# Performance work log

Measured on AMD Instinct MI355X. Metric: run time of the kernel, lower is better.

## Reference

```python
import jax, jax.numpy as jnp
import numpy as np

N_HEADS = 16
HEAD_DIM = 128


def _rotate_half(x):
    x1, x2 = jnp.split(x, 2, axis=-1)
    return jnp.concatenate((-x2, x1), axis=-1)


def setup_inputs() -> dict:
    key = jax.random.key(0)
    ks = jax.random.split(key, 6)
    B, T, D = 2, 2048, 2048
    d = D // N_HEADS  # 128
    x = jax.random.normal(ks[0], (B, T, D), dtype=jnp.float32)
    # RoPE tables (shape [1,1,T,head_dim]) built as in standard implementations
    inv_freq = 1.0 / (10000.0 ** (jnp.arange(0, d, 2, dtype=jnp.float32) / d))
    ang = jnp.arange(T, dtype=jnp.float32)[:, None] * inv_freq[None, :]  # [T, d/2]
    emb = jnp.concatenate((ang, ang), axis=-1)  # [T, d]
    rope_cos = jnp.cos(emb)[None, None]
    rope_sin = jnp.sin(emb)[None, None]
    qkv_w = jax.random.normal(ks[1], (3 * D, D), dtype=jnp.float32) * (1.0 / np.sqrt(D))
    qkv_b = jnp.zeros((3 * D,), dtype=jnp.float32)
    out_w = jax.random.normal(ks[2], (D, D), dtype=jnp.float32) * (1.0 / np.sqrt(D))
    out_b = jnp.zeros((D,), dtype=jnp.float32)
    return {"x": x, "rope_cos": rope_cos, "rope_sin": rope_sin,
            "qkv_w": qkv_w, "qkv_b": qkv_b, "out_w": out_w, "out_b": out_b}


def reference(x, rope_cos, rope_sin, qkv_w, qkv_b, out_w, out_b):
    B, T, D = x.shape
    H, d = N_HEADS, D // N_HEADS
    # fused QKV projection: [B,T,3D] -> [3,B,H,T,d]
    qkv = (jnp.einsum('btd,ed->bte', x, qkv_w) + qkv_b)
    qkv = qkv.reshape(B, T, 3, H, d).transpose(2, 0, 3, 1, 4)
    q, k, v = qkv[0], qkv[1], qkv[2]
    cos = rope_cos[:, :, :T, :].astype(q.dtype)
    sin = rope_sin[:, :, :T, :].astype(q.dtype)
    q = q * cos + _rotate_half(q) * sin
    k = k * cos + _rotate_half(k) * sin
    # causal SDPA
    scale = 1.0 / jnp.sqrt(jnp.array(d, dtype=q.dtype))
    scores = jnp.einsum('bhqd,bhkd->bhqk', q, k) * scale  # [B,H,T,T]
    causal = jnp.tril(jnp.ones((T, T), dtype=bool))
    scores = jnp.where(causal, scores, jnp.finfo(scores.dtype).min)
    attn = jax.nn.softmax(scores, axis=-1)
    out = jnp.einsum('bhqk,bhkd->bhqd', attn, v)  # [B,H,T,d]
    out = out.transpose(0, 2, 1, 3).reshape(B, T, D)
    return jnp.einsum('btd,ed->bte', out, out_w) + out_b
```

## Files before the change

### kernel.cpp

```cpp
#include <hip/hip_runtime.h>
#include <cstdint>
#include <cstddef>

typedef unsigned short u16;
using bf16x8 = __attribute__((ext_vector_type(8))) short;
using f32x4  = __attribute__((ext_vector_type(4))) float;

#define MFMA16(a, b, c) __builtin_amdgcn_mfma_f32_16x16x32_bf16((a), (b), (c), 0, 0, 0)

__device__ __forceinline__ u16 f2bf(float f) {
  union { float f; unsigned u; } x; x.f = f;
  unsigned r = x.u + 0x7fffu + ((x.u >> 16) & 1u);
  return (u16)(r >> 16);
}
__device__ __forceinline__ float bf2f(u16 h) {
  union { unsigned u; float f; } x; x.u = ((unsigned)h) << 16;
  return x.f;
}
__device__ __forceinline__ void gll16(const void* g, void* l) {
  __builtin_amdgcn_global_load_lds((const __attribute__((address_space(1))) void*)g,
                                   (__attribute__((address_space(3))) void*)l, 16, 0, 0);
}

union U8 { bf16x8 v; u16 u[8]; };

__global__ __launch_bounds__(256) void cvt_kernel(const float* __restrict__ in,
                                                  u16* __restrict__ out, int n4) {
  int i = blockIdx.x * blockDim.x + threadIdx.x;
  if (i >= n4) return;
  float4 v = ((const float4*)in)[i];
  ushort4 o;
  o.x = f2bf(v.x); o.y = f2bf(v.y); o.z = f2bf(v.z); o.w = f2bf(v.w);
  ((ushort4*)out)[i] = o;
}

__global__ __launch_bounds__(256) void gemm_bt(const u16* __restrict__ A,
                                               const u16* __restrict__ Bw,
                                               const float* __restrict__ bias,
                                               void* __restrict__ Cout,
                                               int M, int N, int K, int out_bf16) {
  __shared__ u16 As[128 * 32];
  __shared__ u16 Bs[128 * 32];
  const int tid = threadIdx.x;
  const int lane = tid & 63, wave = tid >> 6;
  const int col = lane & 15, quad = lane >> 4;
  const int wr = wave >> 1, wc = wave & 1;
  const int bm = blockIdx.y, bn = blockIdx.x;
  const u16* Ag = A + (size_t)bm * 128 * K;
  const u16* Bg = Bw + (size_t)bn * 128 * K;
  f32x4 acc[4][4] = {};
  const int r0 = tid >> 2, kc = (tid & 3) * 8;
  for (int k0 = 0; k0 < K; k0 += 32) {
    __syncthreads();
    gll16(Ag + (size_t)r0 * K + k0 + kc,        (void*)(As + (size_t)tid * 8));
    gll16(Ag + (size_t)(r0 + 64) * K + k0 + kc, (void*)(As + (size_t)(256 + tid) * 8));
    gll16(Bg + (size_t)r0 * K + k0 + kc,        (void*)(Bs + (size_t)tid * 8));
    gll16(Bg + (size_t)(r0 + 64) * K + k0 + kc, (void*)(Bs + (size_t)(256 + tid) * 8));
    __syncthreads();
    bf16x8 af[4], bf[4];
#pragma unroll
    for (int i = 0; i < 4; i++) {
      af[i] = *(const bf16x8*)&As[(wr * 64 + i * 16 + col) * 32 + quad * 8];
      bf[i] = *(const bf16x8*)&Bs[(wc * 64 + i * 16 + col) * 32 + quad * 8];
    }
#pragma unroll
    for (int i = 0; i < 4; i++)
#pragma unroll
      for (int j = 0; j < 4; j++)
        acc[i][j] = MFMA16(af[i], bf[j], acc[i][j]);
  }
#pragma unroll
  for (int i = 0; i < 4; i++) {
    int row0 = bm * 128 + wr * 64 + i * 16 + quad * 4;
#pragma unroll
    for (int j = 0; j < 4; j++) {
      int cn = bn * 128 + wc * 64 + j * 16 + col;
      float bv = bias[cn];
#pragma unroll
      for (int r = 0; r < 4; r++) {
        float v = acc[i][j][r] + bv;
        size_t off = (size_t)(row0 + r) * N + cn;
        if (out_bf16) ((u16*)Cout)[off] = f2bf(v);
        else          ((float*)Cout)[off] = v;
      }
    }
  }
}

__global__ __launch_bounds__(256) void rope_kernel(const u16* __restrict__ qkv,
                                                   const float* __restrict__ cosT,
                                                   const float* __restrict__ sinT,
                                                   u16* __restrict__ qo,
                                                   u16* __restrict__ ko,
                                                   u16* __restrict__ vt) {
  __shared__ u16 vs[128 * 72];
  const int bh = blockIdx.x;
  const int b = bh >> 4, h = bh & 15;
  const int tb = blockIdx.y;
  const int tid = threadIdx.x;
  const int tl = tid >> 2;
  const int g = tid & 3;
  const int t = tb * 64 + tl;
  const size_t qrow = ((size_t)(b * 2048 + t)) * 6144 + h * 128;
  const size_t orow = ((size_t)bh * 2048 + t) * 128;
  const int tt = t * 128;
  const int dl = g * 16, dh = 64 + dl;
  const float scale = 0.08838834764831845f;
#pragma unroll
  for (int cch = 0; cch < 2; cch++) {
    const int o8 = cch * 8;
    U8 ql, qh, kl, kh, vl, vh;
    ql.v = *(const bf16x8*)&qkv[qrow + dl + o8];
    qh.v = *(const bf16x8*)&qkv[qrow + dh + o8];
    kl.v = *(const bf16x8*)&qkv[qrow + 2048 + dl + o8];
    kh.v = *(const bf16x8*)&qkv[qrow + 2048 + dh + o8];
    vl.v = *(const bf16x8*)&qkv[qrow + 4096 + dl + o8];
    vh.v = *(const bf16x8*)&qkv[qrow + 4096 + dh + o8];
    float cl[8], ch_[8], sl[8], sh_[8];
    *(float4*)&cl[0]  = *(const float4*)&cosT[tt + dl + o8];
    *(float4*)&cl[4]  = *(const float4*)&cosT[tt + dl + o8 + 4];
    *(float4*)&ch_[0] = *(const float4*)&cosT[tt + dh + o8];
    *(float4*)&ch_[4] = *(const float4*)&cosT[tt + dh + o8 + 4];
    *(float4*)&sl[0]  = *(const float4*)&sinT[tt + dl + o8];
    *(float4*)&sl[4]  = *(const float4*)&sinT[tt + dl + o8 + 4];
    *(float4*)&sh_[0] = *(const float4*)&sinT[tt + dh + o8];
    *(float4*)&sh_[4] = *(const float4*)&sinT[tt + dh + o8 + 4];
    U8 aq, bq, ak, bk;
#pragma unroll
    for (int i = 0; i < 8; i++) {
      float qlf = bf2f(ql.u[i]), qhf = bf2f(qh.u[i]);
      float klf = bf2f(kl.u[i]), khf = bf2f(kh.u[i]);
      aq.u[i] = f2bf((qlf * cl[i]  - qhf * sl[i])  * scale);
      bq.u[i] = f2bf((qhf * ch_[i] + qlf * sh_[i]) * scale);
      ak.u[i] = f2bf(klf * cl[i]  - khf * sl[i]);
      bk.u[i] = f2bf(khf * ch_[i] + klf * sh_[i]);
    }
    *(bf16x8*)&qo[orow + dl + o8] = aq.v;
    *(bf16x8*)&qo[orow + dh + o8] = bq.v;
    *(bf16x8*)&ko[orow + dl + o8] = ak.v;
    *(bf16x8*)&ko[orow + dh + o8] = bk.v;
#pragma unroll
    for (int i = 0; i < 8; i++) {
      vs[(dl + o8 + i) * 72 + tl] = vl.u[i];
      vs[(dh + o8 + i) * 72 + tl] = vh.u[i];
    }
  }
  __syncthreads();
#pragma unroll
  for (int c = 0; c < 4; c++) {
    int idx = c * 256 + tid;
    int dd = idx >> 3, chk = idx & 7;
    bf16x8 vv = *(const bf16x8*)&vs[dd * 72 + chk * 8];
    *(bf16x8*)&vt[((size_t)bh * 128 + dd) * 2048 + tb * 64 + chk * 8] = vv;
  }
}

__global__ __launch_bounds__(256) void attn_kernel(const u16* __restrict__ Q,
                                                   const u16* __restrict__ Kk,
                                                   const u16* __restrict__ Vt,
                                                   u16* __restrict__ O) {
  __shared__ u16 Ks[64 * 136];
  __shared__ u16 Vs[128 * 72];
  __shared__ u16 Ps[4][16 * 72];
  const int bh = blockIdx.y, b = bh >> 4, h = bh & 15;
  const int qtile = gridDim.x - 1 - blockIdx.x;
  const int qb = qtile * 128;
  const int tid = threadIdx.x, wave = tid >> 6, lane = tid & 63;
  const int col = lane & 15, quad = lane >> 4;
  const int qw0 = qb + wave * 32;
  const int qw1 = qw0 + 16;
  const u16* Qg = Q + (size_t)bh * 2048 * 128;
  const u16* Kg = Kk + (size_t)bh * 2048 * 128;
  const u16* Vg = Vt + (size_t)bh * 128 * 2048;
  bf16x8 qf0[4], qf1[4];
#pragma unroll
  for (int c = 0; c < 4; c++) {
    qf0[c] = *(const bf16x8*)&Qg[(size_t)(qw0 + col) * 128 + c * 32 + quad * 8];
    qf1[c] = *(const bf16x8*)&Qg[(size_t)(qw1 + col) * 128 + c * 32 + quad * 8];
  }
  f32x4 o0[8] = {}, o1[8] = {};
  float ls0[4] = {0.f, 0.f, 0.f, 0.f}, ls1[4] = {0.f, 0.f, 0.f, 0.f};
  const int ntiles = (qb + 128) >> 6;
  const int kr = tid >> 2, kc = (tid & 3) * 8;
  const int vr = tid >> 1, vc = (tid & 1) * 8;
  for (int it = 0; it < ntiles; ++it) {
    const int kt = it << 6;
    __syncthreads();
#pragma unroll
    for (int u = 0; u < 4; u++)
      *(bf16x8*)&Ks[kr * 136 + kc + u * 32] =
          *(const bf16x8*)&Kg[(size_t)(kt + kr) * 128 + kc + u * 32];
#pragma unroll
    for (int u = 0; u < 4; u++)
      *(bf16x8*)&Vs[vr * 72 + vc + u * 16] =
          *(const bf16x8*)&Vg[(size_t)vr * 2048 + kt + vc + u * 16];
    __syncthreads();
    if (kt > qw1 + 15) continue;
    const bool do0 = (kt <= qw0 + 15);
    f32x4 s0[4] = {}, s1[4] = {};
#pragma unroll
    for (int c = 0; c < 4; c++) {
#pragma unroll
      for (int kg = 0; kg < 4; kg++) {
        bf16x8 kf = *(const bf16x8*)&Ks[(kg * 16 + col) * 136 + c * 32 + quad * 8];
        s0[kg] = MFMA16(qf0[c], kf, s0[kg]);
        s1[kg] = MFMA16(qf1[c], kf, s1[kg]);
      }
    }
    u16* pw = Ps[wave];
    if (do0) {
#pragma unroll
      for (int kg = 0; kg < 4; kg++)
#pragma unroll
        for (int r = 0; r < 4; r++) {
          int key = kt + kg * 16 + col, qg = qw0 + quad * 4 + r;
          float p = (key <= qg) ? __expf(s0[kg][r]) : 0.f;
          ls0[r] += p;
          pw[(quad * 4 + r) * 72 + kg * 16 + col] = f2bf(p);
        }
#pragma unroll
      for (int ks = 0; ks < 64; ks += 32) {
        bf16x8 pf = *(const bf16x8*)&pw[col * 72 + ks + quad * 8];
#pragma unroll
        for (int dt = 0; dt < 8; dt++) {
          bf16x8 vf = *(const bf16x8*)&Vs[(dt * 16 + col) * 72 + ks + quad * 8];
          o0[dt] = MFMA16(pf, vf, o0[dt]);
        }
      }
    }
    {
#pragma unroll
      for (int kg = 0; kg < 4; kg++)
#pragma unroll
        for (int r = 0; r < 4; r++) {
          int key = kt + kg * 16 + col, qg = qw1 + quad * 4 + r;
          float p = (key <= qg) ? __expf(s1[kg][r]) : 0.f;
          ls1[r] += p;
          pw[(quad * 4 + r) * 72 + kg * 16 + col] = f2bf(p);
        }
#pragma unroll
      for (int ks = 0; ks < 64; ks += 32) {
        bf16x8 pf = *(const bf16x8*)&pw[col * 72 + ks + quad * 8];
#pragma unroll
        for (int dt = 0; dt < 8; dt++) {
          bf16x8 vf = *(const bf16x8*)&Vs[(dt * 16 + col) * 72 + ks + quad * 8];
          o1[dt] = MFMA16(pf, vf, o1[dt]);
        }
      }
    }
  }
#pragma unroll
  for (int st = 1; st < 16; st <<= 1)
#pragma unroll
    for (int r = 0; r < 4; r++) {
      ls0[r] += __shfl_xor(ls0[r], st);
      ls1[r] += __shfl_xor(ls1[r], st);
    }
#pragma unroll
  for (int r = 0; r < 4; r++) {
    float inv0 = 1.0f / ls0[r], inv1 = 1.0f / ls1[r];
    size_t row0 = ((size_t)(b * 2048 + qw0 + quad * 4 + r)) * 2048 + h * 128;
    size_t row1 = ((size_t)(b * 2048 + qw1 + quad * 4 + r)) * 2048 + h * 128;
#pragma unroll
    for (int dt = 0; dt < 8; dt++) {
      O[row0 + dt * 16 + col] = f2bf(o0[dt][r] * inv0);
      O[row1 + dt * 16 + col] = f2bf(o1[dt][r] * inv1);
    }
  }
}

extern "C" void kernel_launch(void* const* d_in, const int* in_sizes, int n_in,
                              void* d_out, int out_size, void* d_ws, size_t ws_size,
                              hipStream_t stream) {
  const float* x        = (const float*)d_in[0];
  const float* rope_cos = (const float*)d_in[1];
  const float* rope_sin = (const float*)d_in[2];
  const float* qkv_w    = (const float*)d_in[3];
  const float* qkv_b    = (const float*)d_in[4];
  const float* out_w    = (const float*)d_in[5];
  const float* out_b    = (const float*)d_in[6];
  float* out = (float*)d_out;
  u16* ws = (u16*)d_ws;
  u16* xb    = ws;
  u16* wqkvb = xb + 8388608;
  u16* woutb = wqkvb + 12582912;
  u16* qkvb  = woutb + 4194304;
  u16* qb    = qkvb + 25165824;
  u16* kb    = qb + 8388608;
  u16* vtb   = kb + 8388608;
  u16* attnb = xb;

  cvt_kernel<<<8192, 256, 0, stream>>>(x, xb, 2097152);
  cvt_kernel<<<12288, 256, 0, stream>>>(qkv_w, wqkvb, 3145728);
  cvt_kernel<<<4096, 256, 0, stream>>>(out_w, woutb, 1048576);
  gemm_bt<<<dim3(48, 32), 256, 0, stream>>>(xb, wqkvb, qkv_b, qkvb, 4096, 6144, 2048, 1);
  rope_kernel<<<dim3(32, 32), 256, 0, stream>>>(qkvb, rope_cos, rope_sin, qb, kb, vtb);
  attn_kernel<<<dim3(16, 32), 256, 0, stream>>>(qb, kb, vtb, attnb);
  gemm_bt<<<dim3(16, 32), 256, 0, stream>>>(attnb, woutb, out_b, out, 4096, 2048, 2048, 0);
}
```

Baseline: 470.4 us.

## Rewrite GEMM as 256x256 tile, triple-buffered, swizzled LDS, 8-wave kernel

Result: no change. 473.0 us (+0.6%).

```diff
diff --git a/kernel.cpp b/kernel.cpp
--- a/kernel.cpp
+++ b/kernel.cpp
@@ -34,48 +34,98 @@
   ((ushort4*)out)[i] = o;
 }
 
-__global__ __launch_bounds__(256) void gemm_bt(const u16* __restrict__ A,
-                                               const u16* __restrict__ Bw,
-                                               const float* __restrict__ bias,
-                                               void* __restrict__ Cout,
-                                               int M, int N, int K, int out_bf16) {
-  __shared__ u16 As[128 * 32];
-  __shared__ u16 Bs[128 * 32];
+__global__ __launch_bounds__(512, 2) void gemm_bt256(const u16* __restrict__ A,
+                                                     const u16* __restrict__ Bw,
+                                                     const float* __restrict__ bias,
+                                                     void* __restrict__ Cout,
+                                                     int M, int N, int K, int out_bf16) {
+  __shared__ u16 As[3][8192];
+  __shared__ u16 Bs[3][8192];
   const int tid = threadIdx.x;
   const int lane = tid & 63, wave = tid >> 6;
   const int col = lane & 15, quad = lane >> 4;
-  const int wr = wave >> 1, wc = wave & 1;
+  const int wr = wave >> 2, wc = wave & 3;
   const int bm = blockIdx.y, bn = blockIdx.x;
-  const u16* Ag = A + (size_t)bm * 128 * K;
-  const u16* Bg = Bw + (size_t)bn * 128 * K;
-  f32x4 acc[4][4] = {};
-  const int r0 = tid >> 2, kc = (tid & 3) * 8;
-  for (int k0 = 0; k0 < K; k0 += 32) {
-    __syncthreads();
-    gll16(Ag + (size_t)r0 * K + k0 + kc,        (void*)(As + (size_t)tid * 8));
-    gll16(Ag + (size_t)(r0 + 64) * K + k0 + kc, (void*)(As + (size_t)(256 + tid) * 8));
-    gll16(Bg + (size_t)r0 * K + k0 + kc,        (void*)(Bs + (size_t)tid * 8));
-    gll16(Bg + (size_t)(r0 + 64) * K + k0 + kc, (void*)(Bs + (size_t)(256 + tid) * 8));
-    __syncthreads();
-    bf16x8 af[4], bf[4];
+  const u16* Ag = A + (size_t)bm * 256 * K;
+  const u16* Bg = Bw + (size_t)bn * 256 * K;
+  const int r0 = tid >> 2, r1 = (tid + 512) >> 2;
+  const int sl = tid & 3;
+  const size_t off0 = (size_t)r0 * K + ((sl ^ ((r0 >> 1) & 3)) << 3);
+  const size_t off1 = (size_t)r1 * K + ((sl ^ ((r1 >> 1) & 3)) << 3);
+  f32x4 acc[8][4] = {};
+  const int NT = K >> 5;
+
+#define STAGE_A(buf, k0) do { \
+    gll16(Ag + off0 + (k0), (void*)(As[buf] + tid * 8)); \
+    gll16(Ag + off1 + (k0), (void*)(As[buf] + 4096 + tid * 8)); } while (0)
+#define STAGE_B(buf, k0) do { \
+    gll16(Bg + off0 + (k0), (void*)(Bs[buf] + tid * 8)); \
+    gll16(Bg + off1 + (k0), (void*)(Bs[buf] + 4096 + tid * 8)); } while (0)
+
+  STAGE_A(0, 0); STAGE_B(0, 0);
+  if (NT > 1) {
+    STAGE_A(1, 32); STAGE_B(1, 32);
+    asm volatile("s_waitcnt vmcnt(4)" ::: "memory");
+  } else {
+    asm volatile("s_waitcnt vmcnt(0)" ::: "memory");
+  }
+  __builtin_amdgcn_s_barrier();
+
+  int cur = 0;
+  for (int t = 0; t < NT; ++t) {
+    const u16* Ab = As[cur];
+    const u16* Bb = Bs[cur];
+    int nx2 = cur + 2; if (nx2 >= 3) nx2 -= 3;
+    const bool pf = (t + 2) < NT;
+    const int k2 = (t + 2) << 5;
+    bf16x8 af[4], bfr[4];
 #pragma unroll
     for (int i = 0; i < 4; i++) {
-      af[i] = *(const bf16x8*)&As[(wr * 64 + i * 16 + col) * 32 + quad * 8];
-      bf[i] = *(const bf16x8*)&Bs[(wc * 64 + i * 16 + col) * 32 + quad * 8];
-    }
+      const int row = wr * 128 + i * 16 + col;
+      af[i] = *(const bf16x8*)&Ab[row * 32 + ((quad ^ ((row >> 1) & 3)) << 3)];
+    }
+#pragma unroll
+    for (int j = 0; j < 4; j++) {
+      const int row = wc * 64 + j * 16 + col;
+      bfr[j] = *(const bf16x8*)&Bb[row * 32 + ((quad ^ ((row >> 1) & 3)) << 3)];
+    }
+    if (pf) STAGE_A(nx2, k2);
+    __builtin_amdgcn_s_barrier();
+    __builtin_amdgcn_s_setprio(1);
 #pragma unroll
     for (int i = 0; i < 4; i++)
 #pragma unroll
       for (int j = 0; j < 4; j++)
-        acc[i][j] = MFMA16(af[i], bf[j], acc[i][j]);
-  }
-#pragma unroll
-  for (int i = 0; i < 4; i++) {
-    int row0 = bm * 128 + wr * 64 + i * 16 + quad * 4;
+        acc[i][j] = MFMA16(af[i], bfr[j], acc[i][j]);
+    __builtin_amdgcn_s_setprio(0);
+    __builtin_amdgcn_s_barrier();
+#pragma unroll
+    for (int i = 0; i < 4; i++) {
+      const int row = wr * 128 + (i + 4) * 16 + col;
+      af[i] = *(const bf16x8*)&Ab[row * 32 + ((quad ^ ((row >> 1) & 3)) << 3)];
+    }
+    if (pf) STAGE_B(nx2, k2);
+    __builtin_amdgcn_s_barrier();
+    __builtin_amdgcn_s_setprio(1);
+#pragma unroll
+    for (int i = 0; i < 4; i++)
+#pragma unroll
+      for (int j = 0; j < 4; j++)
+        acc[4 + i][j] = MFMA16(af[i], bfr[j], acc[4 + i][j]);
+    __builtin_amdgcn_s_setprio(0);
+    if (pf) asm volatile("s_waitcnt vmcnt(4)" ::: "memory");
+    else    asm volatile("s_waitcnt vmcnt(0)" ::: "memory");
+    __builtin_amdgcn_s_barrier();
+    cur = (cur + 1 == 3) ? 0 : cur + 1;
+  }
+
+#pragma unroll
+  for (int i = 0; i < 8; i++) {
+    const int row0 = bm * 256 + wr * 128 + i * 16 + quad * 4;
 #pragma unroll
     for (int j = 0; j < 4; j++) {
-      int cn = bn * 128 + wc * 64 + j * 16 + col;
-      float bv = bias[cn];
+      const int cn = bn * 256 + wc * 64 + j * 16 + col;
+      const float bv = bias[cn];
 #pragma unroll
       for (int r = 0; r < 4; r++) {
         float v = acc[i][j][r] + bv;
@@ -85,6 +135,8 @@
       }
     }
   }
+#undef STAGE_A
+#undef STAGE_B
 }
 
 __global__ __launch_bounds__(256) void rope_kernel(const u16* __restrict__ qkv,
@@ -293,8 +345,8 @@
   cvt_kernel<<<8192, 256, 0, stream>>>(x, xb, 2097152);
   cvt_kernel<<<12288, 256, 0, stream>>>(qkv_w, wqkvb, 3145728);
   cvt_kernel<<<4096, 256, 0, stream>>>(out_w, woutb, 1048576);
-  gemm_bt<<<dim3(48, 32), 256, 0, stream>>>(xb, wqkvb, qkv_b, qkvb, 4096, 6144, 2048, 1);
+  gemm_bt256<<<dim3(24, 16), 512, 0, stream>>>(xb, wqkvb, qkv_b, qkvb, 4096, 6144, 2048, 1);
   rope_kernel<<<dim3(32, 32), 256, 0, stream>>>(qkvb, rope_cos, rope_sin, qb, kb, vtb);
   attn_kernel<<<dim3(16, 32), 256, 0, stream>>>(qb, kb, vtb, attnb);
-  gemm_bt<<<dim3(16, 32), 256, 0, stream>>>(attnb, woutb, out_b, out, 4096, 2048, 2048, 0);
-}
+  gemm_bt256<<<dim3(8, 16), 512, 0, stream>>>(attnb, woutb, out_b, out, 4096, 2048, 2048, 0);
+}
```

## Replace GEMM with 256x256-tile, 4-stage pipelined, LDS-swizzled MFMA kernel

Applied to the files above, without the earlier changes.

Measured after the change: 448.8 us. 1.05x faster.

```diff
diff --git a/kernel.cpp b/kernel.cpp
--- a/kernel.cpp
+++ b/kernel.cpp
@@ -34,48 +34,102 @@
   ((ushort4*)out)[i] = o;
 }
 
-__global__ __launch_bounds__(256) void gemm_bt(const u16* __restrict__ A,
-                                               const u16* __restrict__ Bw,
-                                               const float* __restrict__ bias,
-                                               void* __restrict__ Cout,
-                                               int M, int N, int K, int out_bf16) {
-  __shared__ u16 As[128 * 32];
-  __shared__ u16 Bs[128 * 32];
+__global__ __launch_bounds__(512, 2) void gemm_bt256(const u16* __restrict__ A,
+                                                     const u16* __restrict__ Bw,
+                                                     const float* __restrict__ bias,
+                                                     void* __restrict__ Cout,
+                                                     int M, int N, int K, int out_bf16) {
+  __shared__ u16 As[4][8192];
+  __shared__ u16 Bs[4][8192];
   const int tid = threadIdx.x;
   const int lane = tid & 63, wave = tid >> 6;
   const int col = lane & 15, quad = lane >> 4;
-  const int wr = wave >> 1, wc = wave & 1;
+  const int wr = wave >> 2, wc = wave & 3;
   const int bm = blockIdx.y, bn = blockIdx.x;
-  const u16* Ag = A + (size_t)bm * 128 * K;
-  const u16* Bg = Bw + (size_t)bn * 128 * K;
-  f32x4 acc[4][4] = {};
-  const int r0 = tid >> 2, kc = (tid & 3) * 8;
-  for (int k0 = 0; k0 < K; k0 += 32) {
-    __syncthreads();
-    gll16(Ag + (size_t)r0 * K + k0 + kc,        (void*)(As + (size_t)tid * 8));
-    gll16(Ag + (size_t)(r0 + 64) * K + k0 + kc, (void*)(As + (size_t)(256 + tid) * 8));
-    gll16(Bg + (size_t)r0 * K + k0 + kc,        (void*)(Bs + (size_t)tid * 8));
-    gll16(Bg + (size_t)(r0 + 64) * K + k0 + kc, (void*)(Bs + (size_t)(256 + tid) * 8));
-    __syncthreads();
-    bf16x8 af[4], bf[4];
-#pragma unroll
-    for (int i = 0; i < 4; i++) {
-      af[i] = *(const bf16x8*)&As[(wr * 64 + i * 16 + col) * 32 + quad * 8];
-      bf[i] = *(const bf16x8*)&Bs[(wc * 64 + i * 16 + col) * 32 + quad * 8];
-    }
-#pragma unroll
-    for (int i = 0; i < 4; i++)
-#pragma unroll
-      for (int j = 0; j < 4; j++)
-        acc[i][j] = MFMA16(af[i], bf[j], acc[i][j]);
-  }
+  const u16* Ag = A + (size_t)bm * 256 * K;
+  const u16* Bg = Bw + (size_t)bn * 256 * K;
+  const int r0 = tid >> 2, r1 = (tid + 512) >> 2;
+  const int sl = tid & 3;
+  const size_t off0 = (size_t)r0 * K + ((sl ^ ((r0 >> 1) & 3)) << 3);
+  const size_t off1 = (size_t)r1 * K + ((sl ^ ((r1 >> 1) & 3)) << 3);
+  f32x4 acc[8][4] = {};
+  const int NT = K >> 5;
+  int ra1[4], ra2[4], rb[4];
 #pragma unroll
   for (int i = 0; i < 4; i++) {
-    int row0 = bm * 128 + wr * 64 + i * 16 + quad * 4;
+    int r1_ = wr * 128 + i * 16 + col;
+    int r2_ = r1_ + 64;
+    int rb_ = wc * 64 + i * 16 + col;
+    ra1[i] = r1_ * 32 + ((quad ^ ((r1_ >> 1) & 3)) << 3);
+    ra2[i] = r2_ * 32 + ((quad ^ ((r2_ >> 1) & 3)) << 3);
+    rb[i]  = rb_ * 32 + ((quad ^ ((rb_ >> 1) & 3)) << 3);
+  }
+
+#define STAGE_A(bi, k0) do { \
+    gll16(Ag + off0 + (k0), (void*)(As[bi] + tid * 8)); \
+    gll16(Ag + off1 + (k0), (void*)(As[bi] + 4096 + tid * 8)); } while (0)
+#define STAGE_B(bi, k0) do { \
+    gll16(Bg + off0 + (k0), (void*)(Bs[bi] + tid * 8)); \
+    gll16(Bg + off1 + (k0), (void*)(Bs[bi] + 4096 + tid * 8)); } while (0)
+
+#define TILE_STEP(AF, BF, AFN, BFN, TT)                                        \
+  do {                                                                         \
+    const u16* Ab_ = As[(TT) & 3];                                             \
+    _Pragma("unroll")                                                          \
+    for (int i_ = 0; i_ < 4; i_++) af2[i_] = *(const bf16x8*)&Ab_[ra2[i_]];    \
+    if ((TT) + 2 < NT) STAGE_A(((TT) + 2) & 3, ((TT) + 2) << 5);               \
+    __builtin_amdgcn_s_setprio(1);                                             \
+    _Pragma("unroll")                                                          \
+    for (int i_ = 0; i_ < 4; i_++)                                             \
+      _Pragma("unroll")                                                        \
+      for (int j_ = 0; j_ < 4; j_++)                                           \
+        acc[i_][j_] = MFMA16(AF[i_], BF[j_], acc[i_][j_]);                     \
+    __builtin_amdgcn_s_setprio(0);                                             \
+    if ((TT) + 2 < NT) { asm volatile("s_waitcnt vmcnt(2)" ::: "memory"); }    \
+    else               { asm volatile("s_waitcnt vmcnt(0)" ::: "memory"); }    \
+    __builtin_amdgcn_s_barrier();                                              \
+    if ((TT) + 1 < NT) {                                                       \
+      const u16* An_ = As[((TT) + 1) & 3];                                     \
+      const u16* Bn_ = Bs[((TT) + 1) & 3];                                     \
+      _Pragma("unroll")                                                        \
+      for (int i_ = 0; i_ < 4; i_++) {                                         \
+        AFN[i_] = *(const bf16x8*)&An_[ra1[i_]];                               \
+        BFN[i_] = *(const bf16x8*)&Bn_[rb[i_]];                                \
+      }                                                                        \
+    }                                                                          \
+    if ((TT) + 2 < NT) STAGE_B(((TT) + 2) & 3, ((TT) + 2) << 5);               \
+    __builtin_amdgcn_s_setprio(1);                                             \
+    _Pragma("unroll")                                                          \
+    for (int i_ = 0; i_ < 4; i_++)                                             \
+      _Pragma("unroll")                                                        \
+      for (int j_ = 0; j_ < 4; j_++)                                           \
+        acc[4 + i_][j_] = MFMA16(af2[i_], BF[j_], acc[4 + i_][j_]);            \
+    __builtin_amdgcn_s_setprio(0);                                             \
+  } while (0)
+
+  STAGE_A(0, 0); STAGE_B(0, 0); STAGE_A(1, 32);
+  asm volatile("s_waitcnt vmcnt(2)" ::: "memory");
+  __builtin_amdgcn_s_barrier();
+  bf16x8 afX[4], bfX[4], afY[4], bfY[4], af2[4];
+#pragma unroll
+  for (int i = 0; i < 4; i++) {
+    afX[i] = *(const bf16x8*)&As[0][ra1[i]];
+    bfX[i] = *(const bf16x8*)&Bs[0][rb[i]];
+  }
+  STAGE_B(1, 32);
+
+  for (int t = 0; t < NT; t += 2) {
+    TILE_STEP(afX, bfX, afY, bfY, t);
+    TILE_STEP(afY, bfY, afX, bfX, t + 1);
+  }
+
+#pragma unroll
+  for (int i = 0; i < 8; i++) {
+    const int row0 = bm * 256 + wr * 128 + i * 16 + quad * 4;
 #pragma unroll
     for (int j = 0; j < 4; j++) {
-      int cn = bn * 128 + wc * 64 + j * 16 + col;
-      float bv = bias[cn];
+      const int cn = bn * 256 + wc * 64 + j * 16 + col;
+      const float bv = bias[cn];
 #pragma unroll
       for (int r = 0; r < 4; r++) {
         float v = acc[i][j][r] + bv;
@@ -85,6 +139,9 @@
       }
     }
   }
+#undef STAGE_A
+#undef STAGE_B
+#undef TILE_STEP
 }
 
 __global__ __launch_bounds__(256) void rope_kernel(const u16* __restrict__ qkv,
@@ -293,8 +350,8 @@
   cvt_kernel<<<8192, 256, 0, stream>>>(x, xb, 2097152);
   cvt_kernel<<<12288, 256, 0, stream>>>(qkv_w, wqkvb, 3145728);
   cvt_kernel<<<4096, 256, 0, stream>>>(out_w, woutb, 1048576);
-  gemm_bt<<<dim3(48, 32), 256, 0, stream>>>(xb, wqkvb, qkv_b, qkvb, 4096, 6144, 2048, 1);
+  gemm_bt256<<<dim3(24, 16), 512, 0, stream>>>(xb, wqkvb, qkv_b, qkvb, 4096, 6144, 2048, 1);
   rope_kernel<<<dim3(32, 32), 256, 0, stream>>>(qkvb, rope_cos, rope_sin, qb, kb, vtb);
   attn_kernel<<<dim3(16, 32), 256, 0, stream>>>(qb, kb, vtb, attnb);
-  gemm_bt<<<dim3(16, 32), 256, 0, stream>>>(attnb, woutb, out_b, out, 4096, 2048, 2048, 0);
-}
+  gemm_bt256<<<dim3(8, 16), 512, 0, stream>>>(attnb, woutb, out_b, out, 4096, 2048, 2048, 0);
+}
```

## Replace GEMM with 256x256 double-buffered 8-wave pipelined kernel with swizzled LDS

Applied to the files above, without the earlier changes.

Result: faster. 452.4 us (-3.8%).

```diff
diff --git a/kernel.cpp b/kernel.cpp
--- a/kernel.cpp
+++ b/kernel.cpp
@@ -34,48 +34,92 @@
   ((ushort4*)out)[i] = o;
 }
 
-__global__ __launch_bounds__(256) void gemm_bt(const u16* __restrict__ A,
-                                               const u16* __restrict__ Bw,
-                                               const float* __restrict__ bias,
-                                               void* __restrict__ Cout,
-                                               int M, int N, int K, int out_bf16) {
-  __shared__ u16 As[128 * 32];
-  __shared__ u16 Bs[128 * 32];
+__global__ __launch_bounds__(512, 2) void gemm_bt256(const u16* __restrict__ A,
+                                                     const u16* __restrict__ Bw,
+                                                     const float* __restrict__ bias,
+                                                     void* __restrict__ Cout,
+                                                     int M, int N, int K, int out_bf16) {
+  __shared__ u16 As_[2][16384];
+  __shared__ u16 Bs_[2][16384];
   const int tid = threadIdx.x;
   const int lane = tid & 63, wave = tid >> 6;
   const int col = lane & 15, quad = lane >> 4;
-  const int wr = wave >> 1, wc = wave & 1;
+  const int wr = wave >> 2, wc = wave & 3;
   const int bm = blockIdx.y, bn = blockIdx.x;
-  const u16* Ag = A + (size_t)bm * 128 * K;
-  const u16* Bg = Bw + (size_t)bn * 128 * K;
-  f32x4 acc[4][4] = {};
-  const int r0 = tid >> 2, kc = (tid & 3) * 8;
-  for (int k0 = 0; k0 < K; k0 += 32) {
-    __syncthreads();
-    gll16(Ag + (size_t)r0 * K + k0 + kc,        (void*)(As + (size_t)tid * 8));
-    gll16(Ag + (size_t)(r0 + 64) * K + k0 + kc, (void*)(As + (size_t)(256 + tid) * 8));
-    gll16(Bg + (size_t)r0 * K + k0 + kc,        (void*)(Bs + (size_t)tid * 8));
-    gll16(Bg + (size_t)(r0 + 64) * K + k0 + kc, (void*)(Bs + (size_t)(256 + tid) * 8));
-    __syncthreads();
-    bf16x8 af[4], bf[4];
-#pragma unroll
-    for (int i = 0; i < 4; i++) {
-      af[i] = *(const bf16x8*)&As[(wr * 64 + i * 16 + col) * 32 + quad * 8];
-      bf[i] = *(const bf16x8*)&Bs[(wc * 64 + i * 16 + col) * 32 + quad * 8];
-    }
-#pragma unroll
-    for (int i = 0; i < 4; i++)
-#pragma unroll
-      for (int j = 0; j < 4; j++)
-        acc[i][j] = MFMA16(af[i], bf[j], acc[i][j]);
-  }
-#pragma unroll
-  for (int i = 0; i < 4; i++) {
-    int row0 = bm * 128 + wr * 64 + i * 16 + quad * 4;
+  const u16* Ag = A + (size_t)bm * 256 * K;
+  const u16* Bg = Bw + (size_t)bn * 256 * K;
+  const int srow = tid >> 2;
+  const int sslot = tid & 3;
+  const int ssw = (sslot ^ ((srow >> 1) & 3)) << 3;
+  const size_t g0 = (size_t)srow * K + ssw;
+  const size_t g1 = (size_t)(srow + 128) * K + ssw;
+  const int swq = (quad ^ ((col >> 1) & 3)) << 3;
+  const int aro = (wr * 128 + col) * 32 + swq;
+  const int bro = (wc * 64 + col) * 32 + swq;
+  u16* const As0 = &As_[0][0]; u16* const As1 = &As_[1][0];
+  u16* const Bs0 = &Bs_[0][0]; u16* const Bs1 = &Bs_[1][0];
+  f32x4 acc[8][4] = {};
+  bf16x8 a[8], bq[2];
+  const int NI = K >> 7;
+
+#define STG_A(BUF, KS, KT) do { \
+    gll16(Ag + g0 + (KT) + (KS) * 32, (void*)((BUF) + (KS) * 8192 + tid * 8)); \
+    gll16(Ag + g1 + (KT) + (KS) * 32, (void*)((BUF) + (KS) * 8192 + 4096 + tid * 8)); } while (0)
+#define STG_B(BUF, KS, KT) do { \
+    gll16(Bg + g0 + (KT) + (KS) * 32, (void*)((BUF) + (KS) * 8192 + tid * 8)); \
+    gll16(Bg + g1 + (KT) + (KS) * 32, (void*)((BUF) + (KS) * 8192 + 4096 + tid * 8)); } while (0)
+#define RD_A(BUF, KS) do { _Pragma("unroll") \
+    for (int m_ = 0; m_ < 8; m_++) \
+      a[m_] = *(const bf16x8*)&(BUF)[(KS) * 8192 + aro + m_ * 512]; } while (0)
+#define RD_B(BUF, KS, NH) do { _Pragma("unroll") \
+    for (int n_ = 0; n_ < 2; n_++) \
+      bq[n_] = *(const bf16x8*)&(BUF)[(KS) * 8192 + bro + ((NH) * 2 + n_) * 512]; } while (0)
+#define MM(NH) do { _Pragma("unroll") \
+    for (int m_ = 0; m_ < 8; m_++) { _Pragma("unroll") \
+      for (int n_ = 0; n_ < 2; n_++) \
+        acc[m_][(NH) * 2 + n_] = MFMA16(a[m_], bq[n_], acc[m_][(NH) * 2 + n_]); } } while (0)
+#define PH(RDS, STGS, MMS, WT) do { \
+    RDS; STGS; \
+    __builtin_amdgcn_s_barrier(); \
+    asm volatile("s_waitcnt lgkmcnt(0)" ::: "memory"); \
+    __builtin_amdgcn_s_setprio(1); \
+    MMS; \
+    __builtin_amdgcn_s_setprio(0); \
+    WT; \
+    __builtin_amdgcn_s_barrier(); } while (0)
+#define VM6 do { asm volatile("s_waitcnt vmcnt(6)" ::: "memory"); } while (0)
+#define VM0 do { asm volatile("s_waitcnt vmcnt(0)" ::: "memory"); } while (0)
+#define NOPW do { } while (0)
+
+#define ITER(I, LAST) do { \
+    const int kt1_ = ((2 * (I) + 1) << 6), kt2_ = kt1_ + 64, kt3_ = kt2_ + 64; \
+    PH({ RD_A(As0, 0); RD_B(Bs0, 0, 0); }, { STG_B(Bs1, 1, kt1_); },                MM(0), NOPW); \
+    PH({ RD_B(Bs0, 0, 1); },               { if (!(LAST)) STG_A(As0, 0, kt2_); },   MM(1), NOPW); \
+    PH({ RD_A(As0, 1); RD_B(Bs0, 1, 1); }, { if (!(LAST)) STG_B(Bs0, 0, kt2_); },   MM(1), NOPW); \
+    PH({ RD_B(Bs0, 1, 0); },               { if (!(LAST)) STG_A(As0, 1, kt2_); },   MM(0), \
+       if (LAST) { VM0; } else { VM6; }); \
+    PH({ RD_A(As1, 0); RD_B(Bs1, 0, 0); }, { if (!(LAST)) STG_B(Bs0, 1, kt2_); },   MM(0), NOPW); \
+    PH({ RD_B(Bs1, 0, 1); },               { if (!(LAST)) STG_A(As1, 0, kt3_); },   MM(1), NOPW); \
+    PH({ RD_A(As1, 1); RD_B(Bs1, 1, 1); }, { if (!(LAST)) STG_B(Bs1, 0, kt3_); },   MM(1), NOPW); \
+    PH({ RD_B(Bs1, 1, 0); },               { if (!(LAST)) STG_A(As1, 1, kt3_); },   MM(0), \
+       if (!(LAST)) { VM6; }); \
+  } while (0)
+
+  STG_A(As0, 0, 0);  STG_B(Bs0, 0, 0);  STG_A(As0, 1, 0);  STG_B(Bs0, 1, 0);
+  STG_A(As1, 0, 64); STG_B(Bs1, 0, 64); STG_A(As1, 1, 64);
+  VM6;
+  __builtin_amdgcn_s_barrier();
+
+  for (int i = 0; i < NI - 1; ++i) ITER(i, false);
+  ITER(NI - 1, true);
+
+#pragma unroll
+  for (int i = 0; i < 8; i++) {
+    const int row0 = bm * 256 + wr * 128 + i * 16 + quad * 4;
 #pragma unroll
     for (int j = 0; j < 4; j++) {
-      int cn = bn * 128 + wc * 64 + j * 16 + col;
-      float bv = bias[cn];
+      const int cn = bn * 256 + wc * 64 + j * 16 + col;
+      const float bv = bias[cn];
 #pragma unroll
       for (int r = 0; r < 4; r++) {
         float v = acc[i][j][r] + bv;
@@ -85,6 +129,16 @@
       }
     }
   }
+#undef STG_A
+#undef STG_B
+#undef RD_A
+#undef RD_B
+#undef MM
+#undef PH
+#undef VM6
+#undef VM0
+#undef NOPW
+#undef ITER
 }
 
 __global__ __launch_bounds__(256) void rope_kernel(const u16* __restrict__ qkv,
@@ -293,8 +347,8 @@
   cvt_kernel<<<8192, 256, 0, stream>>>(x, xb, 2097152);
   cvt_kernel<<<12288, 256, 0, stream>>>(qkv_w, wqkvb, 3145728);
   cvt_kernel<<<4096, 256, 0, stream>>>(out_w, woutb, 1048576);
-  gemm_bt<<<dim3(48, 32), 256, 0, stream>>>(xb, wqkvb, qkv_b, qkvb, 4096, 6144, 2048, 1);
+  gemm_bt256<<<dim3(24, 16), 512, 0, stream>>>(xb, wqkvb, qkv_b, qkvb, 4096, 6144, 2048, 1);
   rope_kernel<<<dim3(32, 32), 256, 0, stream>>>(qkvb, rope_cos, rope_sin, qb, kb, vtb);
   attn_kernel<<<dim3(16, 32), 256, 0, stream>>>(qb, kb, vtb, attnb);
-  gemm_bt<<<dim3(16, 32), 256, 0, stream>>>(attnb, woutb, out_b, out, 4096, 2048, 2048, 0);
-}
+  gemm_bt256<<<dim3(8, 16), 512, 0, stream>>>(attnb, woutb, out_b, out, 4096, 2048, 2048, 0);
+}
```
